# Optimization experiments

Hardware: AMD Instinct MI355X
Metric: run time of the kernel (lower is better)

## Reference

```python
import math
import jax, jax.numpy as jnp
import numpy as np

KV_SIZE = 960
EPS = 1e-5  # InstanceNorm2d default eps


def _instance_norm(x):
    # x: [B, H, C, K]; InstanceNorm2d(affine=False): normalize each (b,h) plane
    mu = x.mean(axis=(-2, -1), keepdims=True)
    var = x.var(axis=(-2, -1), keepdims=True)  # biased variance, matches torch
    return (x - mu) * jax.lax.rsqrt(var + EPS)


def _branch(emb, Wq, K, V, Wo):
    # emb: [B,N,C], Wq: [H,C,C], K/V: [B,H,N,KV], Wo: [C,C]
    Q = jnp.einsum('bnc,hdc->bhnd', emb, Wq)                       # per-head Linear
    scores = jnp.einsum('bhnc,bhnk->bhck', Q, K) / math.sqrt(KV_SIZE)
    probs = jax.nn.softmax(_instance_norm(scores), axis=-1)        # [B,H,C,KV]
    ctx = jnp.einsum('bhck,bhnk->bhcn', probs, V)                  # [B,H,C,N]
    ctx = ctx.mean(axis=1).transpose(0, 2, 1)                      # mean over heads -> [B,N,C]
    return ctx @ Wo.T                                              # out Linear (no bias)


def setup_inputs() -> dict:
    key = jax.random.key(0)
    ks = jax.random.split(key, 16)
    B, N, H = 8, 1024, 4
    C = [64, 128, 256, 512]
    d = {}
    for i, c in enumerate(C):
        d[f'emb{i+1}'] = jax.random.normal(ks[i], (B, N, c), dtype=jnp.float32)
    d['emb_all'] = jax.random.normal(ks[4], (B, N, KV_SIZE), dtype=jnp.float32)
    for i, c in enumerate(C):
        d[f'Wq{i+1}'] = jax.random.normal(ks[5 + i], (H, c, c), dtype=jnp.float32) * 0.02
    d['Wk'] = jax.random.normal(ks[9], (H, KV_SIZE, KV_SIZE), dtype=jnp.float32) * 0.02
    d['Wv'] = jax.random.normal(ks[10], (H, KV_SIZE, KV_SIZE), dtype=jnp.float32) * 0.02
    for i, c in enumerate(C):
        d[f'Wo{i+1}'] = jax.random.normal(ks[11 + i], (c, c), dtype=jnp.float32) * 0.02
    return d


def reference(emb1, emb2, emb3, emb4, emb_all,
              Wq1, Wq2, Wq3, Wq4, Wk, Wv,
              Wo1, Wo2, Wo3, Wo4):
    # shared K/V: per-head Linear over emb_all -> [B,H,N,KV]
    K = jnp.einsum('bnk,hjk->bhnj', emb_all, Wk)
    V = jnp.einsum('bnk,hjk->bhnj', emb_all, Wv)
    O1 = _branch(emb1, Wq1, K, V, Wo1)
    O2 = _branch(emb2, Wq2, K, V, Wo2)
    O3 = _branch(emb3, Wq3, K, V, Wo3)
    O4 = _branch(emb4, Wq4, K, V, Wo4)
    return (O1, O2, O3, O4)
```

## Files before the change

### kernel.cpp

```cpp
#include <hip/hip_runtime.h>
#include <stdint.h>

typedef unsigned short u16;
typedef short bf16x8 __attribute__((ext_vector_type(8)));
typedef float f32x4 __attribute__((ext_vector_type(4)));
typedef u16 u16x4 __attribute__((ext_vector_type(4)));

__device__ __forceinline__ u16 f2bf(float f) {
    unsigned u = __builtin_bit_cast(unsigned, f);
    unsigned r = (u + 0x7fffu + ((u >> 16) & 1u)) >> 16;
    return (u16)r;
}
__device__ __forceinline__ float bf2f(u16 h) {
    unsigned u = ((unsigned)h) << 16;
    return __builtin_bit_cast(float, u);
}

typedef const __attribute__((address_space(1))) unsigned int* gptr_t;
typedef __attribute__((address_space(3))) unsigned int* lptr_t;
__device__ __forceinline__ void gload16(const void* g, void* l) {
    __builtin_amdgcn_global_load_lds((gptr_t)(uintptr_t)g, (lptr_t)(uintptr_t)l, 16, 0, 0);
}

__device__ __constant__ int d_offs[4] = {0, 512, 768, 896};
__device__ __constant__ int d_cs[4] = {512, 256, 128, 64};

__global__ __launch_bounds__(256) void cast_bf16(const float4* __restrict__ in,
                                                 u16x4* __restrict__ out, int n4) {
    int i = blockIdx.x * 256 + threadIdx.x;
    if (i < n4) {
        float4 f = in[i];
        u16x4 o = {f2bf(f.x), f2bf(f.y), f2bf(f.z), f2bf(f.w)};
        out[i] = o;
    }
}

#define ARDH(DST, BUFO, H)                                                         \
    _Pragma("unroll") for (int f = 0; f < HMF; f++)                                \
        _Pragma("unroll") for (int kb = 0; kb < 2; kb++) {                         \
            int rl = ((H)*HMF + f) * 16 + la;                                      \
            DST[f][kb] = *(const bf16x8*)&lds[(BUFO) + rl * 64 +                   \
                                              (((kb * 4 + lk4) ^ (rl & 7)) << 3)]; \
        }
#define BRD(BUFO)                                                                  \
    _Pragma("unroll") for (int ni = 0; ni < 4; ni++)                               \
        _Pragma("unroll") for (int kb = 0; kb < 2; kb++) {                         \
            int rl = brow0 + ni * 16 + la;                                         \
            breg[ni][kb] = *(const bf16x8*)&lds[(BUFO) + rl * 64 +                 \
                                                (((kb * 4 + lk4) ^ (rl & 7)) << 3)]; \
        }
#define MMAH(H, SRC)                                                               \
    __builtin_amdgcn_sched_barrier(0);                                             \
    __builtin_amdgcn_s_setprio(1);                                                 \
    _Pragma("unroll") for (int f = 0; f < HMF; f++)                                \
        _Pragma("unroll") for (int ni = 0; ni < 4; ni++)                           \
            _Pragma("unroll") for (int kb = 0; kb < 2; kb++)                       \
                acc[(H)*HMF + f][ni] = __builtin_amdgcn_mfma_f32_16x16x32_bf16(    \
                    SRC[f][kb], breg[ni][kb], acc[(H)*HMF + f][ni], 0, 0, 0);      \
    __builtin_amdgcn_s_setprio(0);
#define WLG0 asm volatile("s_waitcnt lgkmcnt(0)" ::: "memory")

template <int BM>
__global__ __launch_bounds__(512, 2) void gemm_nt_4ph(
    const u16* __restrict__ A, long sAb, long sAh, int lda,
    const u16* __restrict__ B, long sBb, long sBh, int ldb,
    u16* __restrict__ C, long sCb, long sCh, int ldc,
    int M, int N, int K, int hdiv, float alpha) {
    constexpr int NA = BM / 128;
    constexpr int WTM = BM / 2;
    constexpr int NMF = WTM / 16;
    constexpr int HMF = NMF / 2;
    constexpr int APART = WTM * 64;
    constexpr int BPART = 128 * 64;
    constexpr int BUFSZ = 2 * APART + 2 * BPART;
    __shared__ u16 lds[2 * BUFSZ];

    int gx = gridDim.x, gy = gridDim.y;
    int nwg = gx * gy * gridDim.z;
    int orig = blockIdx.x + gx * (blockIdx.y + gy * blockIdx.z);
    int q = nwg >> 3, r = nwg & 7;
    int xcd = orig & 7, seq = orig >> 3;
    int wg = (xcd < r ? xcd * (q + 1) : r * (q + 1) + (xcd - r) * q) + seq;
    int bx = wg % gx, tmpw = wg / gx;
    int by = tmpw % gy, bz = tmpw / gy;

    int bb = bz / hdiv, hh = bz - bb * hdiv;
    const u16* Ab = A + (size_t)bb * sAb + (size_t)hh * sAh;
    const u16* Bb = B + (size_t)bb * sBb + (size_t)hh * sBh;
    u16* Cb = C + (size_t)bb * sCb + (size_t)hh * sCh;
    int tm = by * BM, tn = bx * 256;
    int t = threadIdx.x, lane = t & 63, w = t >> 6;
    int wm = w >> 2, wn = w & 3;
    int la = lane & 15, lk4 = lane >> 4;
    int brow0 = (wn & 1) * 64;

    const u16* pA0[NA];
    const u16* pA1[NA];
    const u16* pB0[2];
    const u16* pB1[2];
#pragma unroll
    for (int i = 0; i < NA; i++) {
        int seg = i * 512 + t;
        int col = (((seg & 7) ^ ((seg >> 3) & 7)) << 3);
        int r0 = tm + (seg >> 3);
        if (r0 > M - 1) r0 = M - 1;
        pA0[i] = Ab + (size_t)r0 * lda + col;
        int r1 = tm + WTM + (seg >> 3);
        if (r1 > M - 1) r1 = M - 1;
        pA1[i] = Ab + (size_t)r1 * lda + col;
    }
#pragma unroll
    for (int i = 0; i < 2; i++) {
        int seg = i * 512 + t;
        int col = (((seg & 7) ^ ((seg >> 3) & 7)) << 3);
        int r0 = tn + (seg >> 3);
        if (r0 > N - 1) r0 = N - 1;
        pB0[i] = Bb + (size_t)r0 * ldb + col;
        int r1 = tn + 128 + (seg >> 3);
        if (r1 > N - 1) r1 = N - 1;
        pB1[i] = Bb + (size_t)r1 * ldb + col;
    }

    auto AOF = [&](int buf, int h) { return buf * BUFSZ + h * APART; };
    auto BOF = [&](int buf, int h) { return buf * BUFSZ + 2 * APART + h * BPART; };
    auto stA0 = [&](int buf) {
#pragma unroll
        for (int i = 0; i < NA; i++) {
            gload16(pA0[i], &lds[AOF(buf, 0) + (i * 512 + t) * 8]);
            pA0[i] += 64;
        }
    };
    auto stA1 = [&](int buf) {
#pragma unroll
        for (int i = 0; i < NA; i++) {
            gload16(pA1[i], &lds[AOF(buf, 1) + (i * 512 + t) * 8]);
            pA1[i] += 64;
        }
    };
    auto stB0 = [&](int buf) {
#pragma unroll
        for (int i = 0; i < 2; i++) {
            gload16(pB0[i], &lds[BOF(buf, 0) + (i * 512 + t) * 8]);
            pB0[i] += 64;
        }
    };
    auto stB1 = [&](int buf) {
#pragma unroll
        for (int i = 0; i < 2; i++) {
            gload16(pB1[i], &lds[BOF(buf, 1) + (i * 512 + t) * 8]);
            pB1[i] += 64;
        }
    };

    int nt = K / 64;
    stA0(0);
    stA1(0);
    stB0(0);
    stB1(0);
    if (nt > 1) {
        stB0(1);
        stB1(1);
        asm volatile("s_waitcnt vmcnt(4)" ::: "memory");
    } else {
        asm volatile("s_waitcnt vmcnt(0)" ::: "memory");
    }
    __builtin_amdgcn_s_barrier();

    f32x4 acc[NMF][4] = {};
    bf16x8 breg[4][2];
    bf16x8 aLo[HMF][2], aHi[HMF][2];

    for (int k = 0; k < nt; ++k) {
        int buf = k & 1, nbuf = buf ^ 1;
        int ao = AOF(buf, wm), bo = BOF(buf, wn >> 1);
        bool s1 = (k + 1 < nt), s2 = (k + 2 < nt);
        BRD(bo)
        ARDH(aLo, ao, 0)
        if (s1) {
            stA0(nbuf);
            stA1(nbuf);
        }
        WLG0;
        MMAH(0, aLo)
        ARDH(aHi, ao, 1)
        __builtin_amdgcn_s_barrier();
        if (s2) {
            stB0(buf);
            stB1(buf);
        }
        WLG0;
        MMAH(1, aHi)
        if (s2)
            asm volatile("s_waitcnt vmcnt(4)" ::: "memory");
        else
            asm volatile("s_waitcnt vmcnt(0)" ::: "memory");
        __builtin_amdgcn_s_barrier();
    }
#pragma unroll
    for (int mi = 0; mi < NMF; mi++)
#pragma unroll
        for (int ni = 0; ni < 4; ni++)
#pragma unroll
            for (int r_ = 0; r_ < 4; r_++) {
                int m = tm + wm * WTM + mi * 16 + ((lane >> 4) << 2) + r_;
                int n = tn + wn * 64 + ni * 16 + la;
                if (m < M && n < N)
                    Cb[(size_t)m * ldc + n] = f2bf(acc[mi][ni][r_] * alpha);
            }
}

template <typename OUT>
__global__ __launch_bounds__(256) void gemm_nt128(
    const u16* __restrict__ A, long sAb, long sAh, int lda,
    const u16* __restrict__ B, long sBb, long sBh, int ldb,
    OUT* __restrict__ C, long sCb, long sCh, int ldc,
    int M, int N, int K, int hdiv, float alpha) {
    __shared__ u16 sA[128 * 64];
    __shared__ u16 sB[128 * 64];
    int gx = gridDim.x, gy = gridDim.y;
    int nwg = gx * gy * gridDim.z;
    int orig = blockIdx.x + gx * (blockIdx.y + gy * blockIdx.z);
    int q = nwg >> 3, r = nwg & 7;
    int xcd = orig & 7, seq = orig >> 3;
    int wg = (xcd < r ? xcd * (q + 1) : r * (q + 1) + (xcd - r) * q) + seq;
    int bx = wg % gx, tmpw = wg / gx;
    int by = tmpw % gy, bz = tmpw / gy;

    int bb = bz / hdiv, hh = bz - bb * hdiv;
    const u16* Ab = A + (size_t)bb * sAb + (size_t)hh * sAh;
    const u16* Bb = B + (size_t)bb * sBb + (size_t)hh * sBh;
    OUT* Cb = C + (size_t)bb * sCb + (size_t)hh * sCh;
    int tm = by * 128, tn = bx * 128;
    int t = threadIdx.x, lane = t & 63, w = t >> 6;
    int wr = w >> 1, wc = w & 1;
    int r0 = t >> 3, c0 = (t & 7) * 8;
    const u16* gA[4];
    const u16* gB[4];
#pragma unroll
    for (int i = 0; i < 4; i++) {
        int ar = tm + i * 32 + r0;
        if (ar > M - 1) ar = M - 1;
        gA[i] = Ab + (size_t)ar * lda + c0;
    }
#pragma unroll
    for (int i = 0; i < 4; i++) {
        int br = tn + i * 32 + r0;
        if (br > N - 1) br = N - 1;
        gB[i] = Bb + (size_t)br * ldb + c0;
    }
    f32x4 acc[4][4] = {};
    int la = lane & 15, lk = (lane >> 4) * 8;
    for (int k0 = 0; k0 < K; k0 += 64) {
#pragma unroll
        for (int i = 0; i < 4; i++) {
            gload16(gA[i], &sA[(i * 256 + t) * 8]);
            gA[i] += 64;
        }
#pragma unroll
        for (int i = 0; i < 4; i++) {
            gload16(gB[i], &sB[(i * 256 + t) * 8]);
            gB[i] += 64;
        }
        __syncthreads();
#pragma unroll
        for (int kk = 0; kk < 64; kk += 32) {
            bf16x8 a[4], b[4];
#pragma unroll
            for (int mi = 0; mi < 4; mi++)
                a[mi] = *(const bf16x8*)&sA[(wr * 64 + mi * 16 + la) * 64 + kk + lk];
#pragma unroll
            for (int ni = 0; ni < 4; ni++)
                b[ni] = *(const bf16x8*)&sB[(wc * 64 + ni * 16 + la) * 64 + kk + lk];
#pragma unroll
            for (int mi = 0; mi < 4; mi++)
#pragma unroll
                for (int ni = 0; ni < 4; ni++)
                    acc[mi][ni] = __builtin_amdgcn_mfma_f32_16x16x32_bf16(
                        a[mi], b[ni], acc[mi][ni], 0, 0, 0);
        }
        __syncthreads();
    }
#pragma unroll
    for (int mi = 0; mi < 4; mi++)
#pragma unroll
        for (int ni = 0; ni < 4; ni++)
#pragma unroll
            for (int r_ = 0; r_ < 4; r_++) {
                int m = tm + wr * 64 + mi * 16 + (lane >> 4) * 4 + r_;
                int n = tn + wc * 64 + ni * 16 + la;
                if (m < M && n < N) {
                    float v = acc[mi][ni][r_] * alpha;
                    if constexpr (sizeof(OUT) == 4)
                        Cb[(size_t)m * ldc + n] = v;
                    else
                        Cb[(size_t)m * ldc + n] = f2bf(v);
                }
            }
}

__global__ __launch_bounds__(256) void in_stats1(const u16* __restrict__ sc,
                                                 double* __restrict__ part,
                                                 int G, int mode, int C) {
    int p = blockIdx.y, g = blockIdx.x, t = threadIdx.x;
    size_t base;
    int n8;
    if (mode) {
        int z = p >> 2, i = p & 3;
        base = (size_t)z * 921600 + (size_t)d_offs[i] * 960;
        n8 = d_cs[i] * 120;
    } else {
        base = (size_t)p * C * 960;
        n8 = C * 120;
    }
    const u16* x = sc + base;
    double s = 0.0, q = 0.0;
    for (int i = g * 256 + t; i < n8; i += G * 256) {
        u16x4 a = *(const u16x4*)&x[i * 8];
        u16x4 b = *(const u16x4*)&x[i * 8 + 4];
#pragma unroll
        for (int j = 0; j < 4; j++) {
            float fa = bf2f(a[j]), fb = bf2f(b[j]);
            s += (double)fa + (double)fb;
            q += (double)fa * fa + (double)fb * fb;
        }
    }
#pragma unroll
    for (int o = 32; o; o >>= 1) {
        s += __shfl_down(s, o);
        q += __shfl_down(q, o);
    }
    __shared__ double rs[4], rq[4];
    int w = t >> 6;
    if ((t & 63) == 0) {
        rs[w] = s;
        rq[w] = q;
    }
    __syncthreads();
    if (t == 0) {
        part[2 * ((size_t)p * G + g)] = rs[0] + rs[1] + rs[2] + rs[3];
        part[2 * ((size_t)p * G + g) + 1] = rq[0] + rq[1] + rq[2] + rq[3];
    }
}

__global__ __launch_bounds__(64) void in_stats2(const double* __restrict__ part,
                                                float* __restrict__ stats,
                                                int G, int mode, int C) {
    int p = blockIdx.x, t = threadIdx.x;
    int cnt = (mode ? d_cs[p & 3] : C) * 960;
    double s = 0.0, q = 0.0;
    if (t < G) {
        s = part[2 * ((size_t)p * G + t)];
        q = part[2 * ((size_t)p * G + t) + 1];
    }
#pragma unroll
    for (int o = 32; o; o >>= 1) {
        s += __shfl_down(s, o);
        q += __shfl_down(q, o);
    }
    if (t == 0) {
        float mu = (float)(s / cnt);
        float var = (float)(q / cnt) - mu * mu;
        stats[2 * p] = mu;
        stats[2 * p + 1] = rsqrtf(var + 1e-5f);
    }
}

__global__ __launch_bounds__(256) void norm_softmax_cat(const u16* __restrict__ sc,
                                                        const float* __restrict__ stats,
                                                        u16* __restrict__ prB) {
    int row = blockIdx.x;
    int z = row / 960, c = row - z * 960;
    int i = c < 512 ? 0 : (c < 768 ? 1 : (c < 896 ? 2 : 3));
    int plane = z * 4 + i;
    int b = z >> 2, h = z & 3;
    const u16* x = sc + (size_t)row * 960;
    u16* o = prB + (((size_t)b * 960 + c) * 4 + h) * 960;
    float mu = stats[2 * plane], rs = stats[2 * plane + 1];
    int t = threadIdx.x;
    bool act = t < 240;
    float v[4];
    float mx = -1e30f;
    if (act) {
        u16x4 d = *(const u16x4*)&x[t * 4];
#pragma unroll
        for (int j = 0; j < 4; j++) {
            v[j] = (bf2f(d[j]) - mu) * rs;
            mx = fmaxf(mx, v[j]);
        }
    }
    __shared__ float r1[4], r2[4];
#pragma unroll
    for (int o_ = 32; o_; o_ >>= 1) mx = fmaxf(mx, __shfl_xor(mx, o_));
    int w = t >> 6;
    if ((t & 63) == 0) r1[w] = mx;
    __syncthreads();
    mx = fmaxf(fmaxf(r1[0], r1[1]), fmaxf(r1[2], r1[3]));
    float s = 0.f;
    if (act) {
#pragma unroll
        for (int j = 0; j < 4; j++) {
            v[j] = __expf(v[j] - mx);
            s += v[j];
        }
    }
#pragma unroll
    for (int o_ = 32; o_; o_ >>= 1) s += __shfl_xor(s, o_);
    if ((t & 63) == 0) r2[w] = s;
    __syncthreads();
    s = r2[0] + r2[1] + r2[2] + r2[3];
    float inv = 1.0f / s;
    if (act) {
        u16x4 ov;
#pragma unroll
        for (int j = 0; j < 4; j++) ov[j] = f2bf(v[j] * inv);
        *(u16x4*)&o[t * 4] = ov;
    }
}

__global__ __launch_bounds__(256) void norm_softmax_ip(u16* sc,
                                                       const float* __restrict__ stats,
                                                       int C) {
    int row = blockIdx.x;
    int plane = row / C;
    u16* x = sc + (size_t)row * 960;
    float mu = stats[2 * plane], rs = stats[2 * plane + 1];
    int t = threadIdx.x;
    bool act = t < 240;
    float v[4];
    float mx = -1e30f;
    if (act) {
        u16x4 d = *(const u16x4*)&x[t * 4];
#pragma unroll
        for (int j = 0; j < 4; j++) {
            v[j] = (bf2f(d[j]) - mu) * rs;
            mx = fmaxf(mx, v[j]);
        }
    }
    __shared__ float r1[4], r2[4];
#pragma unroll
    for (int o = 32; o; o >>= 1) mx = fmaxf(mx, __shfl_xor(mx, o));
    int w = t >> 6;
    if ((t & 63) == 0) r1[w] = mx;
    __syncthreads();
    mx = fmaxf(fmaxf(r1[0], r1[1]), fmaxf(r1[2], r1[3]));
    float s = 0.f;
    if (act) {
#pragma unroll
        for (int j = 0; j < 4; j++) {
            v[j] = __expf(v[j] - mx);
            s += v[j];
        }
    }
#pragma unroll
    for (int o = 32; o; o >>= 1) s += __shfl_xor(s, o);
    if ((t & 63) == 0) r2[w] = s;
    __syncthreads();
    s = r2[0] + r2[1] + r2[2] + r2[3];
    float inv = 1.0f / s;
    if (act) {
        u16x4 o;
#pragma unroll
        for (int j = 0; j < 4; j++) o[j] = f2bf(v[j] * inv);
        *(u16x4*)&x[t * 4] = o;
    }
}

__global__ __launch_bounds__(256) void mean_heads(const u16* __restrict__ ctx, long ps,
                                                  u16* __restrict__ cm, int C) {
    int b = blockIdx.z;
    int n0 = blockIdx.x * 64, c0 = blockIdx.y * 64;
    __shared__ float sm[64][65];
    int t = threadIdx.x;
    float acc[16];
#pragma unroll
    for (int j = 0; j < 16; j++) acc[j] = 0.f;
    for (int h = 0; h < 4; h++) {
        const u16* p = ctx + (size_t)(b * 4 + h) * ps;
#pragma unroll
        for (int j = 0; j < 16; j++) {
            int lin = j * 256 + t;
            int cc = lin >> 6, nn = lin & 63;
            acc[j] += bf2f(p[(size_t)(c0 + cc) * 1024 + n0 + nn]);
        }
    }
#pragma unroll
    for (int j = 0; j < 16; j++) {
        int lin = j * 256 + t;
        sm[lin >> 6][lin & 63] = acc[j] * 0.25f;
    }
    __syncthreads();
#pragma unroll
    for (int j = 0; j < 16; j++) {
        int lin = j * 256 + t;
        int nn = lin >> 6, cc = lin & 63;
        cm[((size_t)b * 1024 + n0 + nn) * C + c0 + cc] = f2bf(sm[cc][nn]);
    }
}

extern "C" void kernel_launch(void* const* d_in, const int* in_sizes, int n_in,
                              void* d_out, int out_size, void* d_ws, size_t ws_size,
                              hipStream_t stream) {
    const int B = 8, NN = 1024, KV = 960;
    const int Cs[4] = {64, 128, 256, 512};
    const int ord[4] = {3, 2, 1, 0};
    const int offs[4] = {0, 512, 768, 896};
    const float* emb[4];
    for (int i = 0; i < 4; i++) emb[i] = (const float*)d_in[i];
    const float* embAll = (const float*)d_in[4];
    const float* Wq[4];
    for (int i = 0; i < 4; i++) Wq[i] = (const float*)d_in[5 + i];
    const float* Wk = (const float*)d_in[9];
    const float* Wv = (const float*)d_in[10];
    const float* Wo[4];
    for (int i = 0; i < 4; i++) Wo[i] = (const float*)d_in[11 + i];
    float* out = (float*)d_out;
    size_t outOff[4];
    {
        size_t o = 0;
        for (int i = 0; i < 4; i++) { outOff[i] = o; o += (size_t)B * NN * Cs[i]; }
    }

    const size_t SKV = 62914560;
    const size_t SSC = 58982400;
    const size_t SWQ = 2785280, SWO = 696320, SCM = 8388608;
    const size_t SPART = 131072, SST = 1024;
    const size_t SMALL = SWQ + SWO + SCM + SPART + SST;
    const size_t NEED_BAT = SSC + 3 * SKV + SMALL + 512;

    float invs = 1.0f / sqrtf((float)KV);
    auto g128 = [](int n) { return (n + 127) / 128; };

    if (ws_size >= NEED_BAT) {
        char* p = (char*)d_ws;
        u16* scB = (u16*)p;        p += SSC;
        u16* QtB = (u16*)p;        p += SKV;
        u16* Kt = (u16*)p;         p += SKV;
        u16* VbC = (u16*)p;        p += SKV;
        u16* wq[4];
        for (int i = 0; i < 4; i++) { wq[i] = (u16*)p; p += (size_t)4 * Cs[i] * Cs[i] * 2; }
        u16* wo[4];
        for (int i = 0; i < 4; i++) { wo[i] = (u16*)p; p += (size_t)Cs[i] * Cs[i] * 2; }
        u16* cmX = (u16*)p;        p += SCM;
        double* part = (double*)p; p += SPART;
        float* stats = (float*)p;

        u16* eA = scB;
        u16* wk = (u16*)((char*)scB + 15728640);
        u16* wv = (u16*)((char*)scB + 23101440);
        u16* prB = QtB;
        u16* cmC = scB;

        auto castL = [&](const float* s, u16* d, size_t n) {
            int n4 = (int)(n / 4);
            cast_bf16<<<(n4 + 255) / 256, 256, 0, stream>>>((const float4*)s, (u16x4*)d, n4);
        };
        castL(embAll, eA, (size_t)B * NN * KV);
        castL(Wk, wk, (size_t)4 * KV * KV);
        castL(Wv, wv, (size_t)4 * KV * KV);
        for (int i = 0; i < 4; i++) castL(Wq[i], wq[i], (size_t)4 * Cs[i] * Cs[i]);
        for (int i = 0; i < 4; i++) castL(Wo[i], wo[i], (size_t)Cs[i] * Cs[i]);

        gemm_nt_4ph<256><<<dim3(4, 4, 32), 512, 0, stream>>>(
            wk, 0, (long)KV * KV, KV, eA, (long)NN * KV, 0, KV,
            Kt, 4 * 983040L, 983040L, NN, KV, NN, KV, 4, 1.0f);
        gemm_nt_4ph<256><<<dim3(4, 4, 32), 512, 0, stream>>>(
            eA, (long)NN * KV, 0, KV, wv, 0, (long)KV * KV, KV,
            VbC, (long)NN * 3840, 960L, 3840, NN, KV, KV, 4, 1.0f);

        for (int j = 0; j < 4; j++) {
            int i = ord[j], C = Cs[i];
            castL(emb[i], cmX, (size_t)B * NN * C);
            if (C == 512) {
                gemm_nt_4ph<256><<<dim3(4, 2, 32), 512, 0, stream>>>(
                    wq[i], 0, (long)C * C, C, cmX, (long)NN * C, 0, C,
                    QtB + (size_t)offs[j] * 1024, 4 * 983040L, 983040L, NN,
                    C, NN, C, 4, 1.0f);
            } else {
                gemm_nt128<u16><<<dim3(8, g128(C), 32), 256, 0, stream>>>(
                    wq[i], 0, (long)C * C, C, cmX, (long)NN * C, 0, C,
                    QtB + (size_t)offs[j] * 1024, 4 * 983040L, 983040L, NN,
                    C, NN, C, 4, 1.0f);
            }
        }
        gemm_nt_4ph<256><<<dim3(4, 4, 32), 512, 0, stream>>>(
            QtB, 983040L, 0, NN, Kt, 983040L, 0, NN,
            scB, 921600L, 0, KV, 960, KV, NN, 1, invs);
        in_stats1<<<dim3(16, 128), 256, 0, stream>>>(scB, part, 16, 1, 0);
        in_stats2<<<128, 64, 0, stream>>>(part, stats, 16, 1, 0);
        norm_softmax_cat<<<32 * 960, 256, 0, stream>>>(scB, stats, prB);
        gemm_nt_4ph<128><<<dim3(4, 8, 8), 512, 0, stream>>>(
            VbC, (long)NN * 3840, 0, 3840, prB, (long)960 * 3840, 0, 3840,
            cmC, (long)NN * 960, 0, 960, NN, 960, 3840, 1, 0.25f);
        for (int j = 0; j < 4; j++) {
            int i = ord[j], C = Cs[i];
            gemm_nt128<float><<<dim3(g128(C), 8, 8), 256, 0, stream>>>(
                cmC + offs[j], (long)NN * 960, 0, 960, wo[i], 0, 0, C,
                out + outOff[i], (long)NN * C, 0, C, NN, C, C, 1, 1.0f);
        }
    } else {
        const size_t S1 = 33554432, S2 = 33554432;
        if (ws_size < S1 + S2 + 2 * SKV + SMALL + 512) return;
        char* p = (char*)d_ws;
        char* buf1 = p;            p += S1;
        char* buf2 = p;            p += S2;
        u16* Kt = (u16*)p;         p += SKV;
        u16* Vb = (u16*)p;         p += SKV;
        u16* wq[4];
        for (int i = 0; i < 4; i++) { wq[i] = (u16*)p; p += (size_t)4 * Cs[i] * Cs[i] * 2; }
        u16* wo[4];
        for (int i = 0; i < 4; i++) { wo[i] = (u16*)p; p += (size_t)Cs[i] * Cs[i] * 2; }
        u16* cmX = (u16*)p;        p += SCM;
        double* part = (double*)p; p += SPART;
        float* stats = (float*)p;

        u16* eA = (u16*)buf1;
        u16* wk = (u16*)(buf1 + 15728640);
        u16* wv = (u16*)(buf1 + 23101440);
        u16* sc = (u16*)buf1;
        u16* Qt = (u16*)buf2;
        u16* ctx = (u16*)buf2;

        auto castL = [&](const float* s, u16* d, size_t n) {
            int n4 = (int)(n / 4);
            cast_bf16<<<(n4 + 255) / 256, 256, 0, stream>>>((const float4*)s, (u16x4*)d, n4);
        };
        castL(embAll, eA, (size_t)B * NN * KV);
        castL(Wk, wk, (size_t)4 * KV * KV);
        castL(Wv, wv, (size_t)4 * KV * KV);
        for (int i = 0; i < 4; i++) castL(Wq[i], wq[i], (size_t)4 * Cs[i] * Cs[i]);
        for (int i = 0; i < 4; i++) castL(Wo[i], wo[i], (size_t)Cs[i] * Cs[i]);

        gemm_nt128<u16><<<dim3(8, 8, 32), 256, 0, stream>>>(
            wk, 0, (long)KV * KV, KV, eA, (long)NN * KV, 0, KV,
            Kt, 4 * 983040L, 983040L, NN, KV, NN, KV, 4, 1.0f);
        gemm_nt128<u16><<<dim3(8, 8, 32), 256, 0, stream>>>(
            eA, (long)NN * KV, 0, KV, wv, 0, (long)KV * KV, KV,
            Vb, 4 * 983040L, 983040L, KV, NN, KV, KV, 4, 1.0f);

        for (int i = 0; i < 4; i++) {
            int C = Cs[i];
            castL(emb[i], cmX, (size_t)B * NN * C);
            gemm_nt128<u16><<<dim3(8, g128(C), 32), 256, 0, stream>>>(
                wq[i], 0, (long)C * C, C, cmX, (long)NN * C, 0, C,
                Qt, 4L * C * NN, (long)C * NN, NN, C, NN, C, 4, 1.0f);
            gemm_nt128<u16><<<dim3(8, g128(C), 32), 256, 0, stream>>>(
                Qt, (long)C * NN, 0, NN, Kt, 983040L, 0, NN,
                sc, (long)C * KV, 0, KV, C, KV, NN, 1, invs);
            in_stats1<<<dim3(64, 32), 256, 0, stream>>>(sc, part, 64, 0, C);
            in_stats2<<<32, 64, 0, stream>>>(part, stats, 64, 0, C);
            norm_softmax_ip<<<32 * C, 256, 0, stream>>>(sc, stats, C);
            gemm_nt128<u16><<<dim3(8, g128(C), 32), 256, 0, stream>>>(
                sc, (long)C * KV, 0, KV, Vb, 983040L, 0, KV,
                ctx, (long)C * NN, 0, NN, C, NN, KV, 1, 1.0f);
            mean_heads<<<dim3(16, C / 64, B), 256, 0, stream>>>(
                ctx, (long)C * NN, cmX, C);
            gemm_nt128<float><<<dim3(g128(C), 8, B), 256, 0, stream>>>(
                cmX, (long)NN * C, 0, C, wo[i], 0, 0, C,
                out + outOff[i], (long)NN * C, 0, C, NN, C, C, 1, 1.0f);
        }
    }
}
```

Measured before the change: 454.3 us.

## Batch casts and small GEMMs into grouped launches, fold stats reduction into softmax

Replaces about fifteen separate cast launches with one multi-segment cast kernel, which now also converts all four embeddings up front into scratch space. The three smaller Q-projection GEMMs and the four output-projection GEMMs each become a single grouped launch, with an XCD-aware remap of workgroup index to tile. The in_stats2 kernel is removed, and each softmax row now sums the 16 partial statistics itself. The aim is to cut launch count and tail idle time, at the cost of redundant partial-stat reads in every softmax block and extra scratch usage.

```diff
diff --git a/kernel.cpp b/kernel.cpp
--- a/kernel.cpp
+++ b/kernel.cpp
@@ -32,6 +32,28 @@
         float4 f = in[i];
         u16x4 o = {f2bf(f.x), f2bf(f.y), f2bf(f.z), f2bf(f.w)};
         out[i] = o;
+    }
+}
+
+struct CastPack {
+    const float4* src[15];
+    u16x4* dst[15];
+    int n4[15];
+    int cum[16];
+    int nseg;
+};
+__global__ __launch_bounds__(256) void cast_multi(CastPack p) {
+    int b = blockIdx.x, t = threadIdx.x;
+    int s = 0;
+    while (s + 1 < p.nseg && b >= p.cum[s + 1]) s++;
+    int lb = b - p.cum[s], nb = p.cum[s + 1] - p.cum[s];
+    const float4* src = p.src[s];
+    u16x4* dst = p.dst[s];
+    int n4 = p.n4[s];
+    for (int i = lb * 256 + t; i < n4; i += nb * 256) {
+        float4 f = src[i];
+        u16x4 o = {f2bf(f.x), f2bf(f.y), f2bf(f.z), f2bf(f.w)};
+        dst[i] = o;
     }
 }
 
@@ -298,6 +320,120 @@
             }
 }
 
+struct GSeg {
+    const u16* A; long sAb, sAh; int lda;
+    const u16* B; long sBb, sBh; int ldb;
+    void* Cp; long sCb, sCh; int ldc;
+    int M, N, K, hdiv, gx, gy, isF32;
+    float alpha;
+};
+struct GPack {
+    GSeg s[4];
+    int cum[5];
+    int nseg;
+};
+__global__ __launch_bounds__(256) void gemm_nt128_grp(GPack p) {
+    int nwg = p.cum[p.nseg];
+    int orig = blockIdx.x;
+    int q = nwg >> 3, r = nwg & 7;
+    int xcd = orig & 7, seq = orig >> 3;
+    int wg = (xcd < r ? xcd * (q + 1) : r * (q + 1) + (xcd - r) * q) + seq;
+    int s = 0;
+    while (s + 1 < p.nseg && wg >= p.cum[s + 1]) s++;
+    GSeg g;
+    if (s == 0) g = p.s[0];
+    else if (s == 1) g = p.s[1];
+    else if (s == 2) g = p.s[2];
+    else g = p.s[3];
+    int lm = wg - p.cum[s];
+    int bx = lm % g.gx;
+    int rest = lm / g.gx;
+    int by = rest % g.gy, bz = rest / g.gy;
+
+    __shared__ u16 sA[128 * 64];
+    __shared__ u16 sB[128 * 64];
+    int bb = bz / g.hdiv, hh = bz - bb * g.hdiv;
+    const u16* Ab = g.A + (size_t)bb * g.sAb + (size_t)hh * g.sAh;
+    const u16* Bb = g.B + (size_t)bb * g.sBb + (size_t)hh * g.sBh;
+    int tm = by * 128, tn = bx * 128;
+    int t = threadIdx.x, lane = t & 63, w = t >> 6;
+    int wr = w >> 1, wc = w & 1;
+    int r0 = t >> 3, c0 = (t & 7) * 8;
+    const u16* gA[4];
+    const u16* gB[4];
+#pragma unroll
+    for (int i = 0; i < 4; i++) {
+        int ar = tm + i * 32 + r0;
+        if (ar > g.M - 1) ar = g.M - 1;
+        gA[i] = Ab + (size_t)ar * g.lda + c0;
+    }
+#pragma unroll
+    for (int i = 0; i < 4; i++) {
+        int br = tn + i * 32 + r0;
+        if (br > g.N - 1) br = g.N - 1;
+        gB[i] = Bb + (size_t)br * g.ldb + c0;
+    }
+    f32x4 acc[4][4] = {};
+    int la = lane & 15, lk = (lane >> 4) * 8;
+    for (int k0 = 0; k0 < g.K; k0 += 64) {
+#pragma unroll
+        for (int i = 0; i < 4; i++) {
+            gload16(gA[i], &sA[(i * 256 + t) * 8]);
+            gA[i] += 64;
+        }
+#pragma unroll
+        for (int i = 0; i < 4; i++) {
+            gload16(gB[i], &sB[(i * 256 + t) * 8]);
+            gB[i] += 64;
+        }
+        __syncthreads();
+#pragma unroll
+        for (int kk = 0; kk < 64; kk += 32) {
+            bf16x8 a[4], b[4];
+#pragma unroll
+            for (int mi = 0; mi < 4; mi++)
+                a[mi] = *(const bf16x8*)&sA[(wr * 64 + mi * 16 + la) * 64 + kk + lk];
+#pragma unroll
+            for (int ni = 0; ni < 4; ni++)
+                b[ni] = *(const bf16x8*)&sB[(wc * 64 + ni * 16 + la) * 64 + kk + lk];
+#pragma unroll
+            for (int mi = 0; mi < 4; mi++)
+#pragma unroll
+                for (int ni = 0; ni < 4; ni++)
+                    acc[mi][ni] = __builtin_amdgcn_mfma_f32_16x16x32_bf16(
+                        a[mi], b[ni], acc[mi][ni], 0, 0, 0);
+        }
+        __syncthreads();
+    }
+    if (g.isF32) {
+        float* Cb = (float*)g.Cp + (size_t)bb * g.sCb + (size_t)hh * g.sCh;
+#pragma unroll
+        for (int mi = 0; mi < 4; mi++)
+#pragma unroll
+            for (int ni = 0; ni < 4; ni++)
+#pragma unroll
+                for (int r_ = 0; r_ < 4; r_++) {
+                    int m = tm + wr * 64 + mi * 16 + (lane >> 4) * 4 + r_;
+                    int n = tn + wc * 64 + ni * 16 + la;
+                    if (m < g.M && n < g.N)
+                        Cb[(size_t)m * g.ldc + n] = acc[mi][ni][r_] * g.alpha;
+                }
+    } else {
+        u16* Cb = (u16*)g.Cp + (size_t)bb * g.sCb + (size_t)hh * g.sCh;
+#pragma unroll
+        for (int mi = 0; mi < 4; mi++)
+#pragma unroll
+            for (int ni = 0; ni < 4; ni++)
+#pragma unroll
+                for (int r_ = 0; r_ < 4; r_++) {
+                    int m = tm + wr * 64 + mi * 16 + (lane >> 4) * 4 + r_;
+                    int n = tn + wc * 64 + ni * 16 + la;
+                    if (m < g.M && n < g.N)
+                        Cb[(size_t)m * g.ldc + n] = f2bf(acc[mi][ni][r_] * g.alpha);
+                }
+    }
+}
+
 __global__ __launch_bounds__(256) void in_stats1(const u16* __restrict__ sc,
                                                  double* __restrict__ part,
                                                  int G, int mode, int C) {
@@ -365,17 +501,26 @@
     }
 }
 
-__global__ __launch_bounds__(256) void norm_softmax_cat(const u16* __restrict__ sc,
-                                                        const float* __restrict__ stats,
-                                                        u16* __restrict__ prB) {
+__global__ __launch_bounds__(256) void norm_softmax_cat2(const u16* __restrict__ sc,
+                                                         const double* __restrict__ part,
+                                                         u16* __restrict__ prB) {
     int row = blockIdx.x;
     int z = row / 960, c = row - z * 960;
     int i = c < 512 ? 0 : (c < 768 ? 1 : (c < 896 ? 2 : 3));
     int plane = z * 4 + i;
     int b = z >> 2, h = z & 3;
+    double s2 = 0.0, q2 = 0.0;
+    for (int j = 0; j < 16; j++) {
+        s2 += part[2 * ((size_t)plane * 16 + j)];
+        q2 += part[2 * ((size_t)plane * 16 + j) + 1];
+    }
+    int cnt = d_cs[i] * 960;
+    float mu = (float)(s2 / cnt);
+    float var = (float)(q2 / cnt) - mu * mu;
+    float rs = rsqrtf(var + 1e-5f);
+
     const u16* x = sc + (size_t)row * 960;
     u16* o = prB + (((size_t)b * 960 + c) * 4 + h) * 960;
-    float mu = stats[2 * plane], rs = stats[2 * plane + 1];
     int t = threadIdx.x;
     bool act = t < 240;
     float v[4];
@@ -502,8 +647,7 @@
                               hipStream_t stream) {
     const int B = 8, NN = 1024, KV = 960;
     const int Cs[4] = {64, 128, 256, 512};
-    const int ord[4] = {3, 2, 1, 0};
-    const int offs[4] = {0, 512, 768, 896};
+    const int offsIn[4] = {896, 768, 512, 0};
     const float* emb[4];
     for (int i = 0; i < 4; i++) emb[i] = (const float*)d_in[i];
     const float* embAll = (const float*)d_in[4];
@@ -542,23 +686,46 @@
         for (int i = 0; i < 4; i++) { wo[i] = (u16*)p; p += (size_t)Cs[i] * Cs[i] * 2; }
         u16* cmX = (u16*)p;        p += SCM;
         double* part = (double*)p; p += SPART;
-        float* stats = (float*)p;
+        (void)cmX;
 
         u16* eA = scB;
         u16* wk = (u16*)((char*)scB + 15728640);
         u16* wv = (u16*)((char*)scB + 23101440);
+        u16* embB[4];
+        {
+            size_t eo = 30474240 / 2;
+            for (int i = 0; i < 4; i++) {
+                embB[i] = scB + eo;
+                eo += (size_t)B * NN * Cs[i];
+            }
+        }
         u16* prB = QtB;
         u16* cmC = scB;
 
-        auto castL = [&](const float* s, u16* d, size_t n) {
-            int n4 = (int)(n / 4);
-            cast_bf16<<<(n4 + 255) / 256, 256, 0, stream>>>((const float4*)s, (u16x4*)d, n4);
-        };
-        castL(embAll, eA, (size_t)B * NN * KV);
-        castL(Wk, wk, (size_t)4 * KV * KV);
-        castL(Wv, wv, (size_t)4 * KV * KV);
-        for (int i = 0; i < 4; i++) castL(Wq[i], wq[i], (size_t)4 * Cs[i] * Cs[i]);
-        for (int i = 0; i < 4; i++) castL(Wo[i], wo[i], (size_t)Cs[i] * Cs[i]);
+        {
+            CastPack cp;
+            int ns = 0;
+            auto add = [&](const float* s, u16* d, size_t n) {
+                cp.src[ns] = (const float4*)s;
+                cp.dst[ns] = (u16x4*)d;
+                cp.n4[ns] = (int)(n / 4);
+                ns++;
+            };
+            add(embAll, eA, (size_t)B * NN * KV);
+            add(Wk, wk, (size_t)4 * KV * KV);
+            add(Wv, wv, (size_t)4 * KV * KV);
+            for (int i = 0; i < 4; i++) add(Wq[i], wq[i], (size_t)4 * Cs[i] * Cs[i]);
+            for (int i = 0; i < 4; i++) add(Wo[i], wo[i], (size_t)Cs[i] * Cs[i]);
+            for (int i = 0; i < 4; i++) add(emb[i], embB[i], (size_t)B * NN * Cs[i]);
+            cp.nseg = ns;
+            cp.cum[0] = 0;
+            for (int i = 0; i < ns; i++) {
+                int nb = (cp.n4[i] + 1023) / 1024;
+                if (nb < 1) nb = 1;
+                cp.cum[i + 1] = cp.cum[i] + nb;
+            }
+            cast_multi<<<cp.cum[ns], 256, 0, stream>>>(cp);
+        }
 
         gemm_nt_4ph<256><<<dim3(4, 4, 32), 512, 0, stream>>>(
             wk, 0, (long)KV * KV, KV, eA, (long)NN * KV, 0, KV,
@@ -567,35 +734,50 @@
             eA, (long)NN * KV, 0, KV, wv, 0, (long)KV * KV, KV,
             VbC, (long)NN * 3840, 960L, 3840, NN, KV, KV, 4, 1.0f);
 
-        for (int j = 0; j < 4; j++) {
-            int i = ord[j], C = Cs[i];
-            castL(emb[i], cmX, (size_t)B * NN * C);
-            if (C == 512) {
-                gemm_nt_4ph<256><<<dim3(4, 2, 32), 512, 0, stream>>>(
-                    wq[i], 0, (long)C * C, C, cmX, (long)NN * C, 0, C,
-                    QtB + (size_t)offs[j] * 1024, 4 * 983040L, 983040L, NN,
-                    C, NN, C, 4, 1.0f);
-            } else {
-                gemm_nt128<u16><<<dim3(8, g128(C), 32), 256, 0, stream>>>(
-                    wq[i], 0, (long)C * C, C, cmX, (long)NN * C, 0, C,
-                    QtB + (size_t)offs[j] * 1024, 4 * 983040L, 983040L, NN,
-                    C, NN, C, 4, 1.0f);
+        gemm_nt_4ph<256><<<dim3(4, 2, 32), 512, 0, stream>>>(
+            wq[3], 0, 512L * 512, 512, embB[3], (long)NN * 512, 0, 512,
+            QtB, 4 * 983040L, 983040L, NN, 512, NN, 512, 4, 1.0f);
+        {
+            GPack gp;
+            gp.nseg = 3;
+            gp.cum[0] = 0;
+            for (int i = 0; i < 3; i++) {
+                int C = Cs[i];
+                GSeg& g = gp.s[i];
+                g.A = wq[i]; g.sAb = 0; g.sAh = (long)C * C; g.lda = C;
+                g.B = embB[i]; g.sBb = (long)NN * C; g.sBh = 0; g.ldb = C;
+                g.Cp = (void*)(QtB + (size_t)offsIn[i] * 1024);
+                g.sCb = 4 * 983040L; g.sCh = 983040L; g.ldc = NN;
+                g.M = C; g.N = NN; g.K = C; g.hdiv = 4;
+                g.gx = 8; g.gy = g128(C); g.isF32 = 0; g.alpha = 1.0f;
+                gp.cum[i + 1] = gp.cum[i] + g.gx * g.gy * 32;
             }
+            gemm_nt128_grp<<<gp.cum[3], 256, 0, stream>>>(gp);
         }
         gemm_nt_4ph<256><<<dim3(4, 4, 32), 512, 0, stream>>>(
             QtB, 983040L, 0, NN, Kt, 983040L, 0, NN,
             scB, 921600L, 0, KV, 960, KV, NN, 1, invs);
         in_stats1<<<dim3(16, 128), 256, 0, stream>>>(scB, part, 16, 1, 0);
-        in_stats2<<<128, 64, 0, stream>>>(part, stats, 16, 1, 0);
-        norm_softmax_cat<<<32 * 960, 256, 0, stream>>>(scB, stats, prB);
+        norm_softmax_cat2<<<32 * 960, 256, 0, stream>>>(scB, part, prB);
         gemm_nt_4ph<128><<<dim3(4, 8, 8), 512, 0, stream>>>(
             VbC, (long)NN * 3840, 0, 3840, prB, (long)960 * 3840, 0, 3840,
             cmC, (long)NN * 960, 0, 960, NN, 960, 3840, 1, 0.25f);
-        for (int j = 0; j < 4; j++) {
-            int i = ord[j], C = Cs[i];
-            gemm_nt128<float><<<dim3(g128(C), 8, 8), 256, 0, stream>>>(
-                cmC + offs[j], (long)NN * 960, 0, 960, wo[i], 0, 0, C,
-                out + outOff[i], (long)NN * C, 0, C, NN, C, C, 1, 1.0f);
+        {
+            GPack gp;
+            gp.nseg = 4;
+            gp.cum[0] = 0;
+            for (int i = 0; i < 4; i++) {
+                int C = Cs[i];
+                GSeg& g = gp.s[i];
+                g.A = cmC + offsIn[i]; g.sAb = (long)NN * 960; g.sAh = 0; g.lda = 960;
+                g.B = wo[i]; g.sBb = 0; g.sBh = 0; g.ldb = C;
+                g.Cp = (void*)(out + outOff[i]);
+                g.sCb = (long)NN * C; g.sCh = 0; g.ldc = C;
+                g.M = NN; g.N = C; g.K = C; g.hdiv = 1;
+                g.gx = g128(C); g.gy = 8; g.isF32 = 1; g.alpha = 1.0f;
+                gp.cum[i + 1] = gp.cum[i] + g.gx * g.gy * 8;
+            }
+            gemm_nt128_grp<<<gp.cum[4], 256, 0, stream>>>(gp);
         }
     } else {
         const size_t S1 = 33554432, S2 = 33554432;
```

Result: faster. 401.4 us, median of 4 (-11.6%).
